# Performance work log

Hardware: AMD Instinct MI355X
Metric: run time of the kernel (lower is better)

Reference implementation:

```python
import jax, jax.numpy as jnp
import numpy as np

N_HEADS = 12
B, S, D = 2, 2048, 768
NEG = -1e9


def setup_inputs() -> dict:
    key = jax.random.key(0)
    ks = jax.random.split(key, 7)
    scale = 1.0 / np.sqrt(D)
    Q = jax.random.normal(ks[0], (B, S, D), jnp.float32)
    K = jax.random.normal(ks[1], (B, S, D), jnp.float32)
    V = jax.random.normal(ks[2], (B, S, D), jnp.float32)
    # causal mask, broadcastable over batch and heads; 0 entries are masked out
    mask = jnp.tril(jnp.ones((S, S), jnp.int32))[None, None, :, :]
    Wq = jax.random.normal(ks[3], (D, D), jnp.float32) * scale
    Wk = jax.random.normal(ks[4], (D, D), jnp.float32) * scale
    Wv = jax.random.normal(ks[5], (D, D), jnp.float32) * scale
    Wo = jax.random.normal(ks[6], (D, D), jnp.float32) * scale
    return {"Q": Q, "K": K, "V": V, "mask": mask,
            "Wq": Wq, "Wk": Wk, "Wv": Wv, "Wo": Wo}


def reference(Q, K, V, mask, Wq, Wk, Wv, Wo):
    b, s, d = Q.shape
    h = N_HEADS
    dk = d // h
    # projections (torch nn.Linear: x @ W.T), split heads -> (b, h, s, dk)
    q = (Q @ Wq.T).reshape(b, s, h, dk).transpose(0, 2, 1, 3)
    k = (K @ Wk.T).reshape(b, s, h, dk).transpose(0, 2, 1, 3)
    v = (V @ Wv.T).reshape(b, s, h, dk).transpose(0, 2, 1, 3)
    scores = jnp.einsum('bhqd,bhkd->bhqk', q, k) / jnp.sqrt(jnp.asarray(dk, q.dtype))
    scores = jnp.where(mask == 0, jnp.asarray(NEG, scores.dtype), scores)
    attn = jax.nn.softmax(scores, axis=-1)  # dropout p=0.0 -> identity
    ctx = jnp.einsum('bhqk,bhkd->bhqd', attn, v)
    ctx = ctx.transpose(0, 2, 1, 3).reshape(b, s, d)
    return ctx @ Wo.T
```

## Files before the change

### kernel.cpp

```cpp
#include <hip/hip_runtime.h>
#include <math.h>

#define NH     12
#define BB     2
#define SEQ    2048
#define DMODEL 768
#define DK     64

typedef __attribute__((ext_vector_type(8))) short short8;
typedef __attribute__((ext_vector_type(4))) short short4v;
typedef __attribute__((ext_vector_type(4))) float floatx4;

__device__ __forceinline__ unsigned short f2bf(float x) {
    unsigned u = __builtin_bit_cast(unsigned, x);
    u = (u + 0x7fffu + ((u >> 16) & 1u)) >> 16;
    return (unsigned short)u;
}
__device__ __forceinline__ unsigned short f2bf_fast(float x) {
    unsigned u = __builtin_bit_cast(unsigned, x);
    return (unsigned short)((u + 0x8000u) >> 16);
}

__device__ __forceinline__ void gld_lds16(const ushort* gptr, ushort* lptr) {
    __builtin_amdgcn_global_load_lds(
        (const __attribute__((address_space(1))) unsigned int*)(const void*)gptr,
        (__attribute__((address_space(3))) unsigned int*)(void*)lptr,
        16, 0, 0);
}

#define SI (BB * SEQ * DMODEL)
#define SW (DMODEL * DMODEL)

__global__ __launch_bounds__(256) void cast_all(
    const float* __restrict__ Q, const float* __restrict__ K, const float* __restrict__ V,
    const float* __restrict__ Wq, const float* __restrict__ Wk, const float* __restrict__ Wv,
    const float* __restrict__ Wo,
    ushort* oQ, ushort* oK, ushort* oV, ushort* oWq, ushort* oWk, ushort* oWv, ushort* oWo) {
    long i = (long)(blockIdx.x * 256 + threadIdx.x) * 4;
    const float* src; ushort* dst; long off;
    if      (i < 1L * SI)          { src = Q;  dst = oQ;  off = i; }
    else if (i < 2L * SI)          { src = K;  dst = oK;  off = i - 1L * SI; }
    else if (i < 3L * SI)          { src = V;  dst = oV;  off = i - 2L * SI; }
    else if (i < 3L * SI + SW)     { src = Wq; dst = oWq; off = i - 3L * SI; }
    else if (i < 3L * SI + 2L*SW)  { src = Wk; dst = oWk; off = i - 3L * SI - SW; }
    else if (i < 3L * SI + 3L*SW)  { src = Wv; dst = oWv; off = i - 3L * SI - 2L * SW; }
    else                           { src = Wo; dst = oWo; off = i - 3L * SI - 3L * SW; }
    float4 v = *(const float4*)(src + off);
    ushort4 o;
    o.x = f2bf(v.x); o.y = f2bf(v.y); o.z = f2bf(v.z); o.w = f2bf(v.w);
    *(ushort4*)(dst + off) = o;
}

template<int MODE>
__device__ __forceinline__ void gemm_body(const ushort* __restrict__ A,
                                          const ushort* __restrict__ W,
                                          float* __restrict__ outF,
                                          ushort* __restrict__ outH,
                                          float scale) {
    const int n0 = blockIdx.x * 128;
    const int m0 = blockIdx.y * 128;
    const int tid  = threadIdx.x;
    const int lane = tid & 63;
    const int wv   = tid >> 6;
    const int l15  = lane & 15;
    const int quad = lane >> 4;
    const int wm = (wv >> 1) * 64;
    const int wn = (wv & 1) * 64;

    __shared__ __align__(16) ushort S[2][2][128 * 32];

    const int srow = tid >> 2;
    const int sch  = tid & 3;
    const int schx = sch ^ ((srow >> 1) & 3);
    const int sw2  = (l15 >> 1) & 3;

    floatx4 acc[4][4];
    #pragma unroll
    for (int i = 0; i < 4; ++i)
        #pragma unroll
        for (int j = 0; j < 4; ++j) acc[i][j] = (floatx4)0.f;

    #pragma unroll
    for (int it = 0; it < 2; ++it) {
        const int r = srow + it * 64;
        gld_lds16(A + (size_t)(m0 + r) * DMODEL + schx * 8, &S[0][0][r * 32 + sch * 8]);
        gld_lds16(W + (size_t)(n0 + r) * DMODEL + schx * 8, &S[0][1][r * 32 + sch * 8]);
    }

    for (int t = 0; t < DMODEL / 32; ++t) {
        __syncthreads();
        if (t + 1 < DMODEL / 32) {
            const int k0 = (t + 1) * 32;
            const int bi = (t + 1) & 1;
            #pragma unroll
            for (int it = 0; it < 2; ++it) {
                const int r = srow + it * 64;
                gld_lds16(A + (size_t)(m0 + r) * DMODEL + k0 + schx * 8, &S[bi][0][r * 32 + sch * 8]);
                gld_lds16(W + (size_t)(n0 + r) * DMODEL + k0 + schx * 8, &S[bi][1][r * 32 + sch * 8]);
            }
        }
        const ushort* As  = S[t & 1][0];
        const ushort* Ws2 = S[t & 1][1];
        short8 af[4], bf[4];
        #pragma unroll
        for (int mi = 0; mi < 4; ++mi)
            af[mi] = *(const short8*)&As[(wm + mi * 16 + l15) * 32 + ((quad ^ sw2) * 8)];
        #pragma unroll
        for (int ni = 0; ni < 4; ++ni)
            bf[ni] = *(const short8*)&Ws2[(wn + ni * 16 + l15) * 32 + ((quad ^ sw2) * 8)];
        #pragma unroll
        for (int mi = 0; mi < 4; ++mi)
            #pragma unroll
            for (int ni = 0; ni < 4; ++ni) {
                if (MODE == 2)
                    acc[mi][ni] = __builtin_amdgcn_mfma_f32_16x16x32_bf16(bf[ni], af[mi], acc[mi][ni], 0, 0, 0);
                else
                    acc[mi][ni] = __builtin_amdgcn_mfma_f32_16x16x32_bf16(af[mi], bf[ni], acc[mi][ni], 0, 0, 0);
            }
    }

    #pragma unroll
    for (int mi = 0; mi < 4; ++mi)
        #pragma unroll
        for (int ni = 0; ni < 4; ++ni)
            #pragma unroll
            for (int r = 0; r < 4; ++r) {
                const float v = acc[mi][ni][r] * scale;
                if (MODE == 2) {
                    const int m = m0 + wm + mi * 16 + l15;
                    const int n = n0 + wn + ni * 16 + quad * 4 + r;
                    const int b = m >> 11, s = m & (SEQ - 1);
                    const int h = n >> 6,  dk = n & 63;
                    outH[(((size_t)b * NH + h) * DK + dk) * SEQ + s] = f2bf(v);
                } else {
                    const int m = m0 + wm + mi * 16 + quad * 4 + r;
                    const int n = n0 + wn + ni * 16 + l15;
                    if (MODE == 0) {
                        outF[(size_t)m * DMODEL + n] = v;
                    } else {
                        const int b = m >> 11, s = m & (SEQ - 1);
                        const int h = n >> 6,  dk = n & 63;
                        outH[(((size_t)b * NH + h) * SEQ + s) * DK + dk] = f2bf(v);
                    }
                }
            }
}

#define QSCALE (0.125f * 1.44269504088896f)

__global__ __launch_bounds__(256) void gemm_qkv(
    const ushort* Qb, const ushort* Kb, const ushort* Vb,
    const ushort* Wqb, const ushort* Wkb, const ushort* Wvb,
    ushort* qh, ushort* kh, ushort* vhT) {
    const int z = blockIdx.z;
    if (z == 0)      gemm_body<1>(Qb, Wqb, nullptr, qh,  QSCALE);
    else if (z == 1) gemm_body<1>(Kb, Wkb, nullptr, kh,  1.0f);
    else             gemm_body<2>(Vb, Wvb, nullptr, vhT, 1.0f);
}

__global__ __launch_bounds__(256) void gemm_out(const ushort* A, const ushort* W, float* out) {
    gemm_body<0>(A, W, out, nullptr, 1.0f);
}

#define NITEMS (24 * 32)

__global__ __launch_bounds__(256) void flash_mfma(const ushort* __restrict__ qh,
                                                  const ushort* __restrict__ kh,
                                                  const ushort* __restrict__ vhT,
                                                  ushort* __restrict__ ctx,
                                                  int* __restrict__ counter) {
    const int tid  = threadIdx.x;
    const int lane = tid & 63;
    const int wv   = tid >> 6;
    const int l15  = lane & 15;
    const int quad = lane >> 4;

    __shared__ __align__(16) ushort KV[2][2][64 * 64];
    __shared__ __align__(16) ushort Ps[4][16 * 72];
    __shared__ int wshare;

    const int srow = tid >> 3;
    const int sch  = tid & 7;
    const int schx = sch ^ (srow & 7);
    const int swq  = l15 & 7;

    for (;;) {
        if (tid == 0) wshare = atomicAdd(counter, 1);
        __syncthreads();
        const int w = wshare;
        if (w >= NITEMS) break;
        const int qt = 31 - (w / 24);
        const int bh = w - (w / 24) * 24;
        const int b  = bh / NH, h = bh % NH;
        const int q0 = qt * 64;

        const ushort* kbase = kh  + (size_t)bh * SEQ * DK;
        const ushort* vbase = vhT + (size_t)bh * DK * SEQ;

        short8 q_frag[2];
        {
            const ushort* qp = qh + ((size_t)bh * SEQ + q0 + wv * 16 + l15) * DK;
            q_frag[0] = *(const short8*)(qp + quad * 8);
            q_frag[1] = *(const short8*)(qp + 32 + quad * 8);
        }

        gld_lds16(kbase + (size_t)srow * DK + schx * 8,        &KV[0][0][srow * 64 + sch * 8]);
        gld_lds16(kbase + (size_t)(srow + 32) * DK + schx * 8, &KV[0][0][(srow + 32) * 64 + sch * 8]);
        gld_lds16(vbase + (size_t)srow * SEQ + schx * 8,       &KV[0][1][srow * 64 + sch * 8]);
        gld_lds16(vbase + (size_t)(srow + 32) * SEQ + schx * 8,&KV[0][1][(srow + 32) * 64 + sch * 8]);

        float m_s = -3.0e38f, l_s = 0.f;
        floatx4 o_acc[4];
        #pragma unroll
        for (int d = 0; d < 4; ++d) o_acc[d] = (floatx4)0.f;

        for (int kt = 0; kt <= qt; ++kt) {
            __syncthreads();
            if (kt < qt) {
                const int k0 = (kt + 1) * 64;
                const int bi = (kt + 1) & 1;
                gld_lds16(kbase + (size_t)(k0 + srow) * DK + schx * 8,        &KV[bi][0][srow * 64 + sch * 8]);
                gld_lds16(kbase + (size_t)(k0 + srow + 32) * DK + schx * 8,   &KV[bi][0][(srow + 32) * 64 + sch * 8]);
                gld_lds16(vbase + (size_t)srow * SEQ + k0 + schx * 8,         &KV[bi][1][srow * 64 + sch * 8]);
                gld_lds16(vbase + (size_t)(srow + 32) * SEQ + k0 + schx * 8,  &KV[bi][1][(srow + 32) * 64 + sch * 8]);
            }
            const ushort* Ks  = KV[kt & 1][0];
            const ushort* Vts = KV[kt & 1][1];

            floatx4 s_acc[4];
            #pragma unroll
            for (int nt = 0; nt < 4; ++nt) s_acc[nt] = (floatx4)0.f;
            #pragma unroll
            for (int kc = 0; kc < 2; ++kc)
                #pragma unroll
                for (int nt = 0; nt < 4; ++nt) {
                    short8 kf = *(const short8*)&Ks[(nt * 16 + l15) * 64 + (((kc * 4 + quad) ^ swq) * 8)];
                    s_acc[nt] = __builtin_amdgcn_mfma_f32_16x16x32_bf16(kf, q_frag[kc], s_acc[nt], 0, 0, 0);
                }

            if (kt == qt) {
                const int ql = wv * 16 + l15;
                #pragma unroll
                for (int nt = 0; nt < 4; ++nt)
                    #pragma unroll
                    for (int r = 0; r < 4; ++r)
                        if (nt * 16 + quad * 4 + r > ql) s_acc[nt][r] = -1.0e30f;
            }

            float mx = s_acc[0][0];
            #pragma unroll
            for (int nt = 0; nt < 4; ++nt)
                #pragma unroll
                for (int r = 0; r < 4; ++r) mx = fmaxf(mx, s_acc[nt][r]);
            mx = fmaxf(mx, __shfl_xor(mx, 16));
            mx = fmaxf(mx, __shfl_xor(mx, 32));
            const float mnew = fmaxf(m_s, mx);
            const float al = exp2f(m_s - mnew);
            m_s = mnew;
            float rs = 0.f;
            #pragma unroll
            for (int nt = 0; nt < 4; ++nt) {
                short4v pk;
                #pragma unroll
                for (int r = 0; r < 4; ++r) {
                    const float p = exp2f(s_acc[nt][r] - mnew);
                    rs += p;
                    pk[r] = (short)f2bf_fast(p);
                }
                *(short4v*)&Ps[wv][l15 * 72 + nt * 16 + quad * 4] = pk;
            }
            rs += __shfl_xor(rs, 16);
            rs += __shfl_xor(rs, 32);
            l_s = l_s * al + rs;

            #pragma unroll
            for (int r = 0; r < 4; ++r) {
                const float ar = __shfl(al, quad * 20 + r);
                #pragma unroll
                for (int d = 0; d < 4; ++d) o_acc[d][r] *= ar;
            }

            #pragma unroll
            for (int kc = 0; kc < 2; ++kc) {
                short8 pf = *(const short8*)&Ps[wv][l15 * 72 + kc * 32 + quad * 8];
                #pragma unroll
                for (int dkt = 0; dkt < 4; ++dkt) {
                    short8 vf = *(const short8*)&Vts[(dkt * 16 + l15) * 64 + (((kc * 4 + quad) ^ swq) * 8)];
                    o_acc[dkt] = __builtin_amdgcn_mfma_f32_16x16x32_bf16(pf, vf, o_acc[dkt], 0, 0, 0);
                }
            }
        }

        #pragma unroll
        for (int r = 0; r < 4; ++r) {
            const float lr = __shfl(l_s, quad * 20 + r);
            const float inv = 1.f / lr;
            const int s = q0 + wv * 16 + quad * 4 + r;
            #pragma unroll
            for (int dkt = 0; dkt < 4; ++dkt) {
                const int d = h * DK + dkt * 16 + l15;
                ctx[((size_t)b * SEQ + s) * DMODEL + d] = f2bf(o_acc[dkt][r] * inv);
            }
        }
    }
}

extern "C" void kernel_launch(void* const* d_in, const int* in_sizes, int n_in,
                              void* d_out, int out_size, void* d_ws, size_t ws_size,
                              hipStream_t stream) {
    const float* Q  = (const float*)d_in[0];
    const float* K  = (const float*)d_in[1];
    const float* V  = (const float*)d_in[2];
    const float* Wq = (const float*)d_in[4];
    const float* Wk = (const float*)d_in[5];
    const float* Wv = (const float*)d_in[6];
    const float* Wo = (const float*)d_in[7];

    char* ws = (char*)d_ws;
    const size_t SZ_IN = (size_t)SI * 2;
    const size_t SZ_W  = (size_t)SW * 2;
    ushort* Qbf = (ushort*)(ws);
    ushort* Kbf = (ushort*)(ws + SZ_IN);
    ushort* Vbf = (ushort*)(ws + 2 * SZ_IN);
    ushort* Wqb = (ushort*)(ws + 3 * SZ_IN);
    ushort* Wkb = (ushort*)(ws + 3 * SZ_IN + SZ_W);
    ushort* Wvb = (ushort*)(ws + 3 * SZ_IN + 2 * SZ_W);
    ushort* Wob = (ushort*)(ws + 3 * SZ_IN + 3 * SZ_W);
    ushort* qh  = (ushort*)(ws + 3 * SZ_IN + 4 * SZ_W);
    ushort* kh  = (ushort*)(ws + 4 * SZ_IN + 4 * SZ_W);
    ushort* vhT = (ushort*)(ws + 5 * SZ_IN + 4 * SZ_W);
    int*    ctr = (int*)   (ws + 6 * SZ_IN + 4 * SZ_W);
    ushort* ctx = Qbf;

    dim3 blk(256);
    cast_all<<<dim3((3 * SI + 4 * SW) / 1024), blk, 0, stream>>>(
        Q, K, V, Wq, Wk, Wv, Wo, Qbf, Kbf, Vbf, Wqb, Wkb, Wvb, Wob);
    hipMemsetAsync(ctr, 0, sizeof(int), stream);
    gemm_qkv<<<dim3(6, 32, 3), blk, 0, stream>>>(Qbf, Kbf, Vbf, Wqb, Wkb, Wvb, qh, kh, vhT);
    flash_mfma<<<dim3(768), blk, 0, stream>>>(qh, kh, vhT, ctx, ctr);
    gemm_out<<<dim3(6, 32), blk, 0, stream>>>(ctx, Wob, (float*)d_out);
}
```

Measured before the change: 227.9 us.

## Fuse fp32 activation cast into QKV GEMM and pair query tiles in flash kernel

The separate cast kernel no longer converts Q/K/V. The QKV GEMM now loads fp32 activations into registers and converts them to bf16 before storing to LDS, which avoids a full write and re-read of the bf16 activation copies. The counter reset moves into the weight-cast kernel, replacing a memset call. The flash kernel now runs 512-thread blocks in which two wave groups handle adjacent query tiles and share each K/V tile load, halving the number of work items. The costs are register-staged loads in the GEMM that are no longer async-to-LDS, and idle iterations for the lower tile's group.

```diff
diff --git a/kernel.cpp b/kernel.cpp
--- a/kernel.cpp
+++ b/kernel.cpp
@@ -31,28 +31,25 @@
 #define SI (BB * SEQ * DMODEL)
 #define SW (DMODEL * DMODEL)
 
-__global__ __launch_bounds__(256) void cast_all(
-    const float* __restrict__ Q, const float* __restrict__ K, const float* __restrict__ V,
-    const float* __restrict__ Wq, const float* __restrict__ Wk, const float* __restrict__ Wv,
-    const float* __restrict__ Wo,
-    ushort* oQ, ushort* oK, ushort* oV, ushort* oWq, ushort* oWk, ushort* oWv, ushort* oWo) {
+__global__ __launch_bounds__(256) void cast_w(
+    const float* __restrict__ Wq, const float* __restrict__ Wk,
+    const float* __restrict__ Wv, const float* __restrict__ Wo,
+    ushort* oWq, ushort* oWk, ushort* oWv, ushort* oWo, int* counter) {
+    if (blockIdx.x == 0 && threadIdx.x == 0) *counter = 0;
     long i = (long)(blockIdx.x * 256 + threadIdx.x) * 4;
     const float* src; ushort* dst; long off;
-    if      (i < 1L * SI)          { src = Q;  dst = oQ;  off = i; }
-    else if (i < 2L * SI)          { src = K;  dst = oK;  off = i - 1L * SI; }
-    else if (i < 3L * SI)          { src = V;  dst = oV;  off = i - 2L * SI; }
-    else if (i < 3L * SI + SW)     { src = Wq; dst = oWq; off = i - 3L * SI; }
-    else if (i < 3L * SI + 2L*SW)  { src = Wk; dst = oWk; off = i - 3L * SI - SW; }
-    else if (i < 3L * SI + 3L*SW)  { src = Wv; dst = oWv; off = i - 3L * SI - 2L * SW; }
-    else                           { src = Wo; dst = oWo; off = i - 3L * SI - 3L * SW; }
+    if      (i < 1L * SW) { src = Wq; dst = oWq; off = i; }
+    else if (i < 2L * SW) { src = Wk; dst = oWk; off = i - 1L * SW; }
+    else if (i < 3L * SW) { src = Wv; dst = oWv; off = i - 2L * SW; }
+    else                  { src = Wo; dst = oWo; off = i - 3L * SW; }
     float4 v = *(const float4*)(src + off);
     ushort4 o;
     o.x = f2bf(v.x); o.y = f2bf(v.y); o.z = f2bf(v.z); o.w = f2bf(v.w);
     *(ushort4*)(dst + off) = o;
 }
 
-template<int MODE>
-__device__ __forceinline__ void gemm_body(const ushort* __restrict__ A,
+template<int MODE, bool AF32>
+__device__ __forceinline__ void gemm_body(const void* __restrict__ Av,
                                           const ushort* __restrict__ W,
                                           float* __restrict__ outF,
                                           ushort* __restrict__ outH,
@@ -74,28 +71,57 @@
     const int schx = sch ^ ((srow >> 1) & 3);
     const int sw2  = (l15 >> 1) & 3;
 
+    const ushort* Ab = (const ushort*)Av;
+    const float*  Af = (const float*)Av;
+
     floatx4 acc[4][4];
     #pragma unroll
     for (int i = 0; i < 4; ++i)
         #pragma unroll
         for (int j = 0; j < 4; ++j) acc[i][j] = (floatx4)0.f;
 
+    float4 ar0[2], ar1[2];
     #pragma unroll
     for (int it = 0; it < 2; ++it) {
         const int r = srow + it * 64;
-        gld_lds16(A + (size_t)(m0 + r) * DMODEL + schx * 8, &S[0][0][r * 32 + sch * 8]);
+        if (AF32) {
+            const float* p = Af + (size_t)(m0 + r) * DMODEL + schx * 8;
+            ar0[it] = *(const float4*)p;
+            ar1[it] = *(const float4*)(p + 4);
+        } else {
+            gld_lds16(Ab + (size_t)(m0 + r) * DMODEL + schx * 8, &S[0][0][r * 32 + sch * 8]);
+        }
         gld_lds16(W + (size_t)(n0 + r) * DMODEL + schx * 8, &S[0][1][r * 32 + sch * 8]);
     }
-
-    for (int t = 0; t < DMODEL / 32; ++t) {
+    if (AF32) {
+        #pragma unroll
+        for (int it = 0; it < 2; ++it) {
+            const int r = srow + it * 64;
+            short8 s8;
+            s8[0] = (short)f2bf(ar0[it].x); s8[1] = (short)f2bf(ar0[it].y);
+            s8[2] = (short)f2bf(ar0[it].z); s8[3] = (short)f2bf(ar0[it].w);
+            s8[4] = (short)f2bf(ar1[it].x); s8[5] = (short)f2bf(ar1[it].y);
+            s8[6] = (short)f2bf(ar1[it].z); s8[7] = (short)f2bf(ar1[it].w);
+            *(short8*)&S[0][0][r * 32 + sch * 8] = s8;
+        }
+    }
+
+    const int NS = DMODEL / 32;
+    for (int t = 0; t < NS; ++t) {
         __syncthreads();
-        if (t + 1 < DMODEL / 32) {
+        const int bi = (t + 1) & 1;
+        if (t + 1 < NS) {
             const int k0 = (t + 1) * 32;
-            const int bi = (t + 1) & 1;
             #pragma unroll
             for (int it = 0; it < 2; ++it) {
                 const int r = srow + it * 64;
-                gld_lds16(A + (size_t)(m0 + r) * DMODEL + k0 + schx * 8, &S[bi][0][r * 32 + sch * 8]);
+                if (AF32) {
+                    const float* p = Af + (size_t)(m0 + r) * DMODEL + k0 + schx * 8;
+                    ar0[it] = *(const float4*)p;
+                    ar1[it] = *(const float4*)(p + 4);
+                } else {
+                    gld_lds16(Ab + (size_t)(m0 + r) * DMODEL + k0 + schx * 8, &S[bi][0][r * 32 + sch * 8]);
+                }
                 gld_lds16(W + (size_t)(n0 + r) * DMODEL + k0 + schx * 8, &S[bi][1][r * 32 + sch * 8]);
             }
         }
@@ -117,6 +143,18 @@
                 else
                     acc[mi][ni] = __builtin_amdgcn_mfma_f32_16x16x32_bf16(af[mi], bf[ni], acc[mi][ni], 0, 0, 0);
             }
+        if (AF32 && t + 1 < NS) {
+            #pragma unroll
+            for (int it = 0; it < 2; ++it) {
+                const int r = srow + it * 64;
+                short8 s8;
+                s8[0] = (short)f2bf(ar0[it].x); s8[1] = (short)f2bf(ar0[it].y);
+                s8[2] = (short)f2bf(ar0[it].z); s8[3] = (short)f2bf(ar0[it].w);
+                s8[4] = (short)f2bf(ar1[it].x); s8[5] = (short)f2bf(ar1[it].y);
+                s8[6] = (short)f2bf(ar1[it].z); s8[7] = (short)f2bf(ar1[it].w);
+                *(short8*)&S[bi][0][r * 32 + sch * 8] = s8;
+            }
+        }
     }
 
     #pragma unroll
@@ -149,22 +187,22 @@
 #define QSCALE (0.125f * 1.44269504088896f)
 
 __global__ __launch_bounds__(256) void gemm_qkv(
-    const ushort* Qb, const ushort* Kb, const ushort* Vb,
+    const float* Q, const float* K, const float* V,
     const ushort* Wqb, const ushort* Wkb, const ushort* Wvb,
     ushort* qh, ushort* kh, ushort* vhT) {
     const int z = blockIdx.z;
-    if (z == 0)      gemm_body<1>(Qb, Wqb, nullptr, qh,  QSCALE);
-    else if (z == 1) gemm_body<1>(Kb, Wkb, nullptr, kh,  1.0f);
-    else             gemm_body<2>(Vb, Wvb, nullptr, vhT, 1.0f);
+    if (z == 0)      gemm_body<1, true>(Q, Wqb, nullptr, qh,  QSCALE);
+    else if (z == 1) gemm_body<1, true>(K, Wkb, nullptr, kh,  1.0f);
+    else             gemm_body<2, true>(V, Wvb, nullptr, vhT, 1.0f);
 }
 
 __global__ __launch_bounds__(256) void gemm_out(const ushort* A, const ushort* W, float* out) {
-    gemm_body<0>(A, W, out, nullptr, 1.0f);
-}
-
-#define NITEMS (24 * 32)
-
-__global__ __launch_bounds__(256) void flash_mfma(const ushort* __restrict__ qh,
+    gemm_body<0, false>(A, W, out, nullptr, 1.0f);
+}
+
+#define NITEMS (24 * 16)
+
+__global__ __launch_bounds__(512) void flash_mfma(const ushort* __restrict__ qh,
                                                   const ushort* __restrict__ kh,
                                                   const ushort* __restrict__ vhT,
                                                   ushort* __restrict__ ctx,
@@ -172,11 +210,12 @@
     const int tid  = threadIdx.x;
     const int lane = tid & 63;
     const int wv   = tid >> 6;
+    const int grp  = wv >> 2;
     const int l15  = lane & 15;
     const int quad = lane >> 4;
 
     __shared__ __align__(16) ushort KV[2][2][64 * 64];
-    __shared__ __align__(16) ushort Ps[4][16 * 72];
+    __shared__ __align__(16) ushort Ps[8][16 * 72];
     __shared__ int wshare;
 
     const int srow = tid >> 3;
@@ -189,41 +228,40 @@
         __syncthreads();
         const int w = wshare;
         if (w >= NITEMS) break;
-        const int qt = 31 - (w / 24);
+        const int qp = 15 - (w / 24);
         const int bh = w - (w / 24) * 24;
         const int b  = bh / NH, h = bh % NH;
+        const int qt = 2 * qp + grp;
         const int q0 = qt * 64;
+        const int ktmax = 2 * qp + 1;
 
         const ushort* kbase = kh  + (size_t)bh * SEQ * DK;
         const ushort* vbase = vhT + (size_t)bh * DK * SEQ;
 
         short8 q_frag[2];
         {
-            const ushort* qp = qh + ((size_t)bh * SEQ + q0 + wv * 16 + l15) * DK;
-            q_frag[0] = *(const short8*)(qp + quad * 8);
-            q_frag[1] = *(const short8*)(qp + 32 + quad * 8);
-        }
-
-        gld_lds16(kbase + (size_t)srow * DK + schx * 8,        &KV[0][0][srow * 64 + sch * 8]);
-        gld_lds16(kbase + (size_t)(srow + 32) * DK + schx * 8, &KV[0][0][(srow + 32) * 64 + sch * 8]);
-        gld_lds16(vbase + (size_t)srow * SEQ + schx * 8,       &KV[0][1][srow * 64 + sch * 8]);
-        gld_lds16(vbase + (size_t)(srow + 32) * SEQ + schx * 8,&KV[0][1][(srow + 32) * 64 + sch * 8]);
+            const ushort* qp_ = qh + ((size_t)bh * SEQ + q0 + (wv & 3) * 16 + l15) * DK;
+            q_frag[0] = *(const short8*)(qp_ + quad * 8);
+            q_frag[1] = *(const short8*)(qp_ + 32 + quad * 8);
+        }
+
+        gld_lds16(kbase + (size_t)srow * DK + schx * 8,  &KV[0][0][srow * 64 + sch * 8]);
+        gld_lds16(vbase + (size_t)srow * SEQ + schx * 8, &KV[0][1][srow * 64 + sch * 8]);
 
         float m_s = -3.0e38f, l_s = 0.f;
         floatx4 o_acc[4];
         #pragma unroll
         for (int d = 0; d < 4; ++d) o_acc[d] = (floatx4)0.f;
 
-        for (int kt = 0; kt <= qt; ++kt) {
+        for (int kt = 0; kt <= ktmax; ++kt) {
             __syncthreads();
-            if (kt < qt) {
+            if (kt < ktmax) {
                 const int k0 = (kt + 1) * 64;
                 const int bi = (kt + 1) & 1;
-                gld_lds16(kbase + (size_t)(k0 + srow) * DK + schx * 8,        &KV[bi][0][srow * 64 + sch * 8]);
-                gld_lds16(kbase + (size_t)(k0 + srow + 32) * DK + schx * 8,   &KV[bi][0][(srow + 32) * 64 + sch * 8]);
-                gld_lds16(vbase + (size_t)srow * SEQ + k0 + schx * 8,         &KV[bi][1][srow * 64 + sch * 8]);
-                gld_lds16(vbase + (size_t)(srow + 32) * SEQ + k0 + schx * 8,  &KV[bi][1][(srow + 32) * 64 + sch * 8]);
-            }
+                gld_lds16(kbase + (size_t)(k0 + srow) * DK + schx * 8, &KV[bi][0][srow * 64 + sch * 8]);
+                gld_lds16(vbase + (size_t)srow * SEQ + k0 + schx * 8,  &KV[bi][1][srow * 64 + sch * 8]);
+            }
+            if (kt > qt) continue;
             const ushort* Ks  = KV[kt & 1][0];
             const ushort* Vts = KV[kt & 1][1];
 
@@ -239,7 +277,7 @@
                 }
 
             if (kt == qt) {
-                const int ql = wv * 16 + l15;
+                const int ql = (wv & 3) * 16 + l15;
                 #pragma unroll
                 for (int nt = 0; nt < 4; ++nt)
                     #pragma unroll
@@ -295,7 +333,7 @@
         for (int r = 0; r < 4; ++r) {
             const float lr = __shfl(l_s, quad * 20 + r);
             const float inv = 1.f / lr;
-            const int s = q0 + wv * 16 + quad * 4 + r;
+            const int s = q0 + (wv & 3) * 16 + quad * 4 + r;
             #pragma unroll
             for (int dkt = 0; dkt < 4; ++dkt) {
                 const int d = h * DK + dkt * 16 + l15;
@@ -319,24 +357,20 @@
     char* ws = (char*)d_ws;
     const size_t SZ_IN = (size_t)SI * 2;
     const size_t SZ_W  = (size_t)SW * 2;
-    ushort* Qbf = (ushort*)(ws);
-    ushort* Kbf = (ushort*)(ws + SZ_IN);
-    ushort* Vbf = (ushort*)(ws + 2 * SZ_IN);
-    ushort* Wqb = (ushort*)(ws + 3 * SZ_IN);
-    ushort* Wkb = (ushort*)(ws + 3 * SZ_IN + SZ_W);
-    ushort* Wvb = (ushort*)(ws + 3 * SZ_IN + 2 * SZ_W);
-    ushort* Wob = (ushort*)(ws + 3 * SZ_IN + 3 * SZ_W);
-    ushort* qh  = (ushort*)(ws + 3 * SZ_IN + 4 * SZ_W);
-    ushort* kh  = (ushort*)(ws + 4 * SZ_IN + 4 * SZ_W);
-    ushort* vhT = (ushort*)(ws + 5 * SZ_IN + 4 * SZ_W);
-    int*    ctr = (int*)   (ws + 6 * SZ_IN + 4 * SZ_W);
-    ushort* ctx = Qbf;
+    ushort* Wqb = (ushort*)(ws);
+    ushort* Wkb = (ushort*)(ws + SZ_W);
+    ushort* Wvb = (ushort*)(ws + 2 * SZ_W);
+    ushort* Wob = (ushort*)(ws + 3 * SZ_W);
+    ushort* qh  = (ushort*)(ws + 4 * SZ_W);
+    ushort* kh  = (ushort*)(ws + 4 * SZ_W + SZ_IN);
+    ushort* vhT = (ushort*)(ws + 4 * SZ_W + 2 * SZ_IN);
+    ushort* ctx = (ushort*)(ws + 4 * SZ_W + 3 * SZ_IN);
+    int*    ctr = (int*)   (ws + 4 * SZ_W + 4 * SZ_IN);
 
     dim3 blk(256);
-    cast_all<<<dim3((3 * SI + 4 * SW) / 1024), blk, 0, stream>>>(
-        Q, K, V, Wq, Wk, Wv, Wo, Qbf, Kbf, Vbf, Wqb, Wkb, Wvb, Wob);
-    hipMemsetAsync(ctr, 0, sizeof(int), stream);
-    gemm_qkv<<<dim3(6, 32, 3), blk, 0, stream>>>(Qbf, Kbf, Vbf, Wqb, Wkb, Wvb, qh, kh, vhT);
-    flash_mfma<<<dim3(768), blk, 0, stream>>>(qh, kh, vhT, ctx, ctr);
+    cast_w<<<dim3(4 * SW / 1024), blk, 0, stream>>>(Wq, Wk, Wv, Wo,
+                                                    Wqb, Wkb, Wvb, Wob, ctr);
+    gemm_qkv<<<dim3(6, 32, 3), blk, 0, stream>>>(Q, K, V, Wqb, Wkb, Wvb, qh, kh, vhT);
+    flash_mfma<<<dim3(768), dim3(512), 0, stream>>>(qh, kh, vhT, ctx, ctr);
     gemm_out<<<dim3(6, 32), blk, 0, stream>>>(ctx, Wob, (float*)d_out);
 }
```

Result: slower. 234.0 us (+2.7%).
